# Kernel tuning notes

Hardware: AMD Instinct MI355X
Metric: run time of the kernel (lower is better)

The kernel has to match this reference:

```python
import jax, jax.numpy as jnp
import numpy as np

N = 50000
E = 800000
IN_DIM = 64
HID = 64
HEADS = 4
D = HID * HEADS  # 256
EPS = 1e-5
NEG_SLOPE = 0.2  # PyG GATConv default LeakyReLU slope


def setup_inputs() -> dict:
    key = jax.random.key(0)
    ks = jax.random.split(key, 16)
    def nrm(k, shape, s=0.05):
        return jax.random.normal(k, shape, dtype=jnp.float32) * s
    x = jax.random.normal(ks[0], (N, IN_DIM), dtype=jnp.float32)
    edge_index = jax.random.randint(ks[1], (2, E), 0, N)
    return {
        "x": x,
        "edge_index": edge_index,
        # layer 0: in=64 -> heads=4, out=64, concat -> 256
        "W0": nrm(ks[2], (IN_DIM, D)),
        "as0": nrm(ks[3], (HEADS, HID)),
        "ad0": nrm(ks[4], (HEADS, HID)),
        "b0": jnp.zeros((D,), jnp.float32),
        # layer 1: in=256 -> heads=4, out=64, concat -> 256
        "W1": nrm(ks[5], (D, D)),
        "as1": nrm(ks[6], (HEADS, HID)),
        "ad1": nrm(ks[7], (HEADS, HID)),
        "b1": jnp.zeros((D,), jnp.float32),
        # layer 2: in=256 -> heads=1, out=1, mean (concat=False)
        "W2": nrm(ks[8], (D, 1)),
        "as2": nrm(ks[9], (1, 1)),
        "ad2": nrm(ks[10], (1, 1)),
        "b2": jnp.zeros((1,), jnp.float32),
        # shared LayerNorm over 256 features
        "ln_g": jnp.ones((D,), jnp.float32),
        "ln_b": jnp.zeros((D,), jnp.float32),
    }


def _gat_conv(x, src, dst, W, a_src, a_dst, bias, concat):
    """PyG-style GATConv (self-loops already appended to src/dst)."""
    n = x.shape[0]
    H, C = a_src.shape
    h = (x @ W).reshape(n, H, C)                # [N,H,C]
    s = (h * a_src[None]).sum(-1)               # [N,H] per-node source score
    t = (h * a_dst[None]).sum(-1)               # [N,H] per-node target score
    e = jax.nn.leaky_relu(s[src] + t[dst], NEG_SLOPE)  # [E,H]
    # segment softmax over incoming edges of each destination node
    m = jax.ops.segment_max(e, dst, num_segments=n)    # [N,H]
    ex = jnp.exp(e - m[dst])
    den = jax.ops.segment_sum(ex, dst, num_segments=n)
    alpha = ex / den[dst]                       # [E,H]
    msg = h[src] * alpha[:, :, None]            # [E,H,C] gather + weight
    out = jax.ops.segment_sum(msg, dst, num_segments=n)  # [N,H,C] scatter-add
    out = out.reshape(n, H * C) if concat else out.mean(axis=1)
    return out + bias


def _layer_norm(x, g, b):
    mu = x.mean(-1, keepdims=True)
    var = ((x - mu) ** 2).mean(-1, keepdims=True)
    return (x - mu) / jnp.sqrt(var + EPS) * g + b


def reference(x, edge_index, W0, as0, ad0, b0, W1, as1, ad1, b1,
              W2, as2, ad2, b2, ln_g, ln_b):
    n = x.shape[0]
    loops = jnp.arange(n, dtype=edge_index.dtype)
    src = jnp.concatenate([edge_index[0], loops])
    dst = jnp.concatenate([edge_index[1], loops])
    h = _gat_conv(x, src, dst, W0, as0, ad0, b0, True)
    h = jax.nn.elu(_layer_norm(h, ln_g, ln_b))
    h = _gat_conv(h, src, dst, W1, as1, ad1, b1, True)
    h = jax.nn.elu(_layer_norm(h, ln_g, ln_b))
    out = _gat_conv(h, src, dst, W2, as2, ad2, b2, False)  # [N,1]
    return out
```

## Files before the change

kernel.cpp:

```cpp
#include <hip/hip_runtime.h>
#include <math.h>

constexpr float NEG_SLOPE = 0.2f;
constexpr float LN_EPS = 1e-5f;

typedef __attribute__((ext_vector_type(8))) short short8;
typedef __attribute__((ext_vector_type(4))) float f32x4;
typedef __attribute__((ext_vector_type(2))) float f32x2;

__device__ inline ushort f2bf(float f) {
    uint u = __float_as_uint(f);
    u += 0x7fffu + ((u >> 16) & 1u);
    return (ushort)(u >> 16);
}

__device__ inline float pick4(float4 v, int h) {
    float r = v.x;
    r = (h == 1) ? v.y : r;
    r = (h == 2) ? v.z : r;
    r = (h == 3) ? v.w : r;
    return r;
}

__device__ inline uchar f2q(float v) {
    int r = __builtin_amdgcn_cvt_pk_fp8_f32(v, v, 0, false);
    return (uchar)(r & 0xff);
}

__device__ inline void fma8q(const uint2& u, float q, f32x2 acc[4]) {
    f32x2 qq = {q, q};
    acc[0] += qq * __builtin_amdgcn_cvt_pk_f32_fp8(u.x, false);
    acc[1] += qq * __builtin_amdgcn_cvt_pk_f32_fp8(u.x, true);
    acc[2] += qq * __builtin_amdgcn_cvt_pk_f32_fp8(u.y, false);
    acc[3] += qq * __builtin_amdgcn_cvt_pk_f32_fp8(u.y, true);
}


__global__ void k_pre(const float* __restrict__ x,
                      const float* __restrict__ W0,
                      const float* __restrict__ W1,
                      ushort* __restrict__ Xb,
                      ushort* __restrict__ Wt0,
                      ushort* __restrict__ Wt1, int N) {
    int i = blockIdx.x * blockDim.x + threadIdx.x;
    const int nx = N * 8;
    if (i < nx) {
        float4 a = *reinterpret_cast<const float4*>(x + (size_t)i * 8);
        float4 b = *reinterpret_cast<const float4*>(x + (size_t)i * 8 + 4);
        ushort u[8] = {f2bf(a.x), f2bf(a.y), f2bf(a.z), f2bf(a.w),
                       f2bf(b.x), f2bf(b.y), f2bf(b.z), f2bf(b.w)};
        *reinterpret_cast<uint4*>(Xb + (size_t)i * 8) = *reinterpret_cast<const uint4*>(u);
        return;
    }
    i -= nx;
    if (i < 64 * 256) {
        int k = i >> 8, c = i & 255;
        Wt0[(size_t)c * 64 + k] = f2bf(W0[i]);
        return;
    }
    i -= 64 * 256;
    if (i < 256 * 256) {
        int k = i >> 8, c = i & 255;
        Wt1[(size_t)c * 256 + k] = f2bf(W1[i]);
    }
}


__global__ __launch_bounds__(1024) void k_cnt(const int* __restrict__ ei, int E, int N,
                                              int* __restrict__ bcnts) {
    __shared__ int lcnt[256];
    const int tid = threadIdx.x;
    if (tid < 256) lcnt[tid] = 0;
    __syncthreads();
    int i = blockIdx.x * 1024 + tid;
    if (i < E + N) {
        int dst = (i < E) ? ei[E + i] : (i - E);
        atomicAdd(&lcnt[dst >> 8], 1);
    }
    __syncthreads();
    if (tid < 256) bcnts[(size_t)blockIdx.x * 256 + tid] = lcnt[tid];
}

__global__ __launch_bounds__(256) void k_scanA(int* __restrict__ bcnts, int nb,
                                               int* __restrict__ wtot) {
    __shared__ int wsum[4];
    const int w = blockIdx.x;
    const int t = threadIdx.x;
    const int lane = t & 63;
    const int wv = t >> 6;
    int carry = 0;
    for (int base = 0; base < nb; base += 256) {
        int idx = base + t;
        int v = (idx < nb) ? bcnts[(size_t)idx * 256 + w] : 0;
        int sv = v;
#pragma unroll
        for (int off = 1; off < 64; off <<= 1) {
            int u = __shfl_up(sv, off);
            if (lane >= off) sv += u;
        }
        if (lane == 63) wsum[wv] = sv;
        __syncthreads();
        int add = 0;
#pragma unroll
        for (int k = 0; k < 4; ++k) add += (k < wv) ? wsum[k] : 0;
        int total = wsum[0] + wsum[1] + wsum[2] + wsum[3];
        if (idx < nb) bcnts[(size_t)idx * 256 + w] = carry + add + sv - v;
        carry += total;
        __syncthreads();
    }
    if (t == 0) wtot[w] = carry;
}

__global__ __launch_bounds__(256) void k_scanB(const int* __restrict__ wtot,
                                               int* __restrict__ wbase, int nbw) {
    __shared__ int buf[256];
    const int t = threadIdx.x;
    int v = (t < nbw) ? wtot[t] : 0;
    buf[t] = v;
    __syncthreads();
    for (int off = 1; off < 256; off <<= 1) {
        int a = (t >= off) ? buf[t - off] : 0;
        __syncthreads();
        buf[t] += a;
        __syncthreads();
    }
    if (t < nbw) wbase[t] = buf[t] - v;
}

__global__ __launch_bounds__(1024) void k_binA(const int* __restrict__ ei, int E, int N,
                                               const int* __restrict__ bcnts,
                                               const int* __restrict__ wbase,
                                               unsigned long long* __restrict__ tmp) {
    __shared__ int lcnt[256];
    __shared__ int lbase[256];
    const int tid = threadIdx.x;
    if (tid < 256) lcnt[tid] = 0;
    __syncthreads();
    int i = blockIdx.x * 1024 + tid;
    int src = 0, dst = 0, rank = 0, buc = 0;
    const bool valid = i < E + N;
    if (valid) {
        if (i < E) { src = ei[i]; dst = ei[E + i]; }
        else       { src = i - E; dst = i - E; }
        buc = dst >> 8;
        rank = atomicAdd(&lcnt[buc], 1);
    }
    __syncthreads();
    if (tid < 256)
        lbase[tid] = wbase[tid] + bcnts[(size_t)blockIdx.x * 256 + tid];
    __syncthreads();
    if (valid)
        tmp[lbase[buc] + rank] = ((unsigned long long)(uint)dst << 32) | (uint)src;
}

__global__ __launch_bounds__(256) void k_win(const unsigned long long* __restrict__ tmp,
                                             const int* __restrict__ wbase,
                                             const int* __restrict__ wtot,
                                             int nbw, int N,
                                             int* __restrict__ offs,
                                             int* __restrict__ csr) {
    __shared__ int hist[256];
    __shared__ int cur[256];
    __shared__ int buf[256];
    const int w = blockIdx.x;
    const int t = threadIdx.x;
    const int base = wbase[w];
    const int count = wtot[w];

    hist[t] = 0;
    __syncthreads();
    for (int i = t; i < count; i += 256) {
        int dst = (int)(tmp[base + i] >> 32);
        atomicAdd(&hist[dst & 255], 1);
    }
    __syncthreads();
    int v = hist[t];
    buf[t] = v;
    __syncthreads();
    for (int off = 1; off < 256; off <<= 1) {
        int a = (t >= off) ? buf[t - off] : 0;
        __syncthreads();
        buf[t] += a;
        __syncthreads();
    }
    int excl = buf[t] - v;
    cur[t] = excl;
    int node = w * 256 + t;
    if (node < N) offs[node] = base + excl;
    if (t == 0 && w == nbw - 1) offs[N] = base + count;
    __syncthreads();
    for (int i = t; i < count; i += 256) {
        unsigned long long e = tmp[base + i];
        int dst = (int)(e >> 32);
        int src = (int)(e & 0xffffffffu);
        int pos = base + atomicAdd(&cur[dst & 255], 1);
        csr[pos] = src;
    }
}


template <int K>
__global__ __launch_bounds__(256, 2) void k_gemm_mfma(
    const ushort* __restrict__ Xb, const ushort* __restrict__ Wt,
    const float* __restrict__ a_s, const float* __restrict__ a_d,
    uchar* __restrict__ h, float* __restrict__ s, float* __restrict__ t,
    int N, int nrb, int cpx, int rbpc)
{
    constexpr int KC = K / 32;
    __shared__ uchar hstage[4][16][72];

    const int tid = threadIdx.x;
    const int w = tid >> 6;
    const int l = tid & 63;
    const int lr = l & 15;
    const int lk = l >> 4;

    const int bid = blockIdx.x;
    const int xcd = bid & 7;
    const int j = bid >> 3;
    const int slice = j & 3;
    const int chunk = xcd * cpx + (j >> 2);
    const int rb0 = chunk * rbpc;
    const int rb1 = min(rb0 + rbpc, nrb);

    short8 b[4][KC];
#pragma unroll
    for (int ct = 0; ct < 4; ++ct) {
        const ushort* wp = Wt + (size_t)(slice * 64 + ct * 16 + lr) * K + lk * 8;
#pragma unroll
        for (int kc = 0; kc < KC; ++kc)
            b[ct][kc] = *reinterpret_cast<const short8*>(wp + kc * 32);
    }

    float asv[4], adv[4];
#pragma unroll
    for (int ct = 0; ct < 4; ++ct) {
        asv[ct] = a_s[slice * 64 + ct * 16 + lr];
        adv[ct] = a_d[slice * 64 + ct * 16 + lr];
    }

    for (int rb = rb0; rb < rb1; ++rb) {
        const int row0 = rb * 64 + w * 16;

        int arow = row0 + lr;
        arow = (arow < N) ? arow : (N - 1);
        const ushort* xp = Xb + (size_t)arow * K + lk * 8;
        short8 a[KC];
#pragma unroll
        for (int kc = 0; kc < KC; ++kc)
            a[kc] = *reinterpret_cast<const short8*>(xp + kc * 32);

        f32x4 acc[4];
#pragma unroll
        for (int ct = 0; ct < 4; ++ct) acc[ct] = (f32x4){0.f, 0.f, 0.f, 0.f};
#pragma unroll
        for (int ct = 0; ct < 4; ++ct)
#pragma unroll
            for (int kc = 0; kc < KC; ++kc)
                acc[ct] = __builtin_amdgcn_mfma_f32_16x16x32_bf16(a[kc], b[ct][kc], acc[ct], 0, 0, 0);

        float ps[4] = {0.f, 0.f, 0.f, 0.f}, pt[4] = {0.f, 0.f, 0.f, 0.f};
#pragma unroll
        for (int jj = 0; jj < 4; ++jj) {
#pragma unroll
            for (int ct = 0; ct < 4; ++ct) {
                float v = acc[ct][jj];
                ps[jj] = fmaf(v, asv[ct], ps[jj]);
                pt[jj] = fmaf(v, adv[ct], pt[jj]);
            }
        }
#pragma unroll
        for (int jj = 0; jj < 4; ++jj) {
#pragma unroll
            for (int o = 1; o < 16; o <<= 1) {
                ps[jj] += __shfl_xor(ps[jj], o);
                pt[jj] += __shfl_xor(pt[jj], o);
            }
        }
        if (lr == 0) {
#pragma unroll
            for (int jj = 0; jj < 4; ++jj) {
                int row = row0 + lk * 4 + jj;
                if (row < N) {
                    s[(size_t)row * 4 + slice] = ps[jj];
                    t[(size_t)row * 4 + slice] = pt[jj];
                }
            }
        }

#pragma unroll
        for (int ct = 0; ct < 4; ++ct)
#pragma unroll
            for (int jj = 0; jj < 4; ++jj)
                hstage[w][lk * 4 + jj][ct * 16 + lr] = f2q(acc[ct][jj]);
#pragma unroll
        for (int hf = 0; hf < 2; ++hf) {
            int r = (l >> 3) + hf * 8;
            int ch = l & 7;
            int grow = rb * 64 + w * 16 + r;
            uint2 v = *reinterpret_cast<const uint2*>(&hstage[w][r][ch * 8]);
            if (grow < N)
                *reinterpret_cast<uint2*>(h + (size_t)grow * 256 + slice * 64 + ch * 8) = v;
        }
    }
}


template <bool FUSE_W2>
__global__ __launch_bounds__(256) void k_agg_ln_elu(
    const int* __restrict__ offs, const int* __restrict__ csr,
    const float* __restrict__ s, const float* __restrict__ t,
    const uchar* __restrict__ h, const float* __restrict__ bias,
    const float* __restrict__ lng, const float* __restrict__ lnb,
    ushort* __restrict__ Y, const float* __restrict__ W2,
    float* __restrict__ h2, int N)
{
    __shared__ float p_s[4][2][32][4];
    __shared__ int off_s[4][2][32];

    const int tid = threadIdx.x;
    const int wid = tid >> 6;
    const int lane = tid & 63;
    const int half = lane >> 5;
    const int lh = lane & 31;
    const int n = blockIdx.x * 8 + wid * 2 + half;
    if (n >= N) return;
    const int head = lh >> 3;
    const int c0 = lh * 8;

    const float4 t4 = *reinterpret_cast<const float4*>(t + (size_t)n * 4);
    const int beg = offs[n], end = offs[n + 1];

    float4 m4 = make_float4(-1e30f, -1e30f, -1e30f, -1e30f);
    float4 den4 = make_float4(0.f, 0.f, 0.f, 0.f);
    f32x2 acc2[4];
#pragma unroll
    for (int c = 0; c < 4; ++c) acc2[c] = (f32x2){0.f, 0.f};

    const uchar* hb = h + lh * 8;
    float* pp = &p_s[wid][half][0][0];
    int* op = &off_s[wid][half][0];

    for (int base = beg; base < end; base += 32) {
        const int cnt = min(32, end - base);
        int src = 0;
        float4 e4 = make_float4(-1e30f, -1e30f, -1e30f, -1e30f);
        if (lh < cnt) {
            src = csr[base + lh];
            float4 sv = *reinterpret_cast<const float4*>(s + (size_t)src * 4);
            float ex = sv.x + t4.x, ey = sv.y + t4.y, ez = sv.z + t4.z, ew = sv.w + t4.w;
            e4.x = fmaxf(ex, NEG_SLOPE * ex);
            e4.y = fmaxf(ey, NEG_SLOPE * ey);
            e4.z = fmaxf(ez, NEG_SLOPE * ez);
            e4.w = fmaxf(ew, NEG_SLOPE * ew);
        }
        float4 bm = e4;
#pragma unroll
        for (int off = 1; off < 32; off <<= 1) {
            bm.x = fmaxf(bm.x, __shfl_xor(bm.x, off));
            bm.y = fmaxf(bm.y, __shfl_xor(bm.y, off));
            bm.z = fmaxf(bm.z, __shfl_xor(bm.z, off));
            bm.w = fmaxf(bm.w, __shfl_xor(bm.w, off));
        }
        float4 newm = make_float4(fmaxf(m4.x, bm.x), fmaxf(m4.y, bm.y),
                                  fmaxf(m4.z, bm.z), fmaxf(m4.w, bm.w));
        float4 sc4 = make_float4(__expf(m4.x - newm.x), __expf(m4.y - newm.y),
                                 __expf(m4.z - newm.z), __expf(m4.w - newm.w));
        m4 = newm;
        float sch = pick4(sc4, head);
        f32x2 sch2 = {sch, sch};
#pragma unroll
        for (int c = 0; c < 4; ++c) acc2[c] *= sch2;
        float4 p4 = make_float4(__expf(e4.x - newm.x), __expf(e4.y - newm.y),
                                __expf(e4.z - newm.z), __expf(e4.w - newm.w));
        den4.x = den4.x * sc4.x + p4.x;
        den4.y = den4.y * sc4.y + p4.y;
        den4.z = den4.z * sc4.z + p4.z;
        den4.w = den4.w * sc4.w + p4.w;

        *reinterpret_cast<float4*>(&p_s[wid][half][lh][0]) = p4;
        op[lh] = src << 8;
        asm volatile("s_waitcnt lgkmcnt(0)" ::: "memory");

        for (int j0 = 0; j0 < cnt; j0 += 4) {
            int o0 = op[j0 + 0];
            int o1 = op[j0 + 1];
            int o2 = op[j0 + 2];
            int o3 = op[j0 + 3];
            float q0 = pp[(j0 + 0) * 4 + head];
            float q1 = pp[(j0 + 1) * 4 + head];
            float q2 = pp[(j0 + 2) * 4 + head];
            float q3 = pp[(j0 + 3) * 4 + head];
            uint2 u0 = *reinterpret_cast<const uint2*>(hb + o0);
            uint2 u1 = *reinterpret_cast<const uint2*>(hb + o1);
            uint2 u2 = *reinterpret_cast<const uint2*>(hb + o2);
            uint2 u3 = *reinterpret_cast<const uint2*>(hb + o3);
            fma8q(u0, q0, acc2);
            fma8q(u1, q1, acc2);
            fma8q(u2, q2, acc2);
            fma8q(u3, q3, acc2);
        }
    }

    float4 dsum = den4;
#pragma unroll
    for (int off = 1; off < 32; off <<= 1) {
        dsum.x += __shfl_xor(dsum.x, off);
        dsum.y += __shfl_xor(dsum.y, off);
        dsum.z += __shfl_xor(dsum.z, off);
        dsum.w += __shfl_xor(dsum.w, off);
    }
    const float inv = 1.0f / pick4(dsum, head);
    float4 bv0 = *reinterpret_cast<const float4*>(bias + c0);
    float4 bv1 = *reinterpret_cast<const float4*>(bias + c0 + 4);
    float v[8];
    v[0] = acc2[0][0] * inv + bv0.x; v[1] = acc2[0][1] * inv + bv0.y;
    v[2] = acc2[1][0] * inv + bv0.z; v[3] = acc2[1][1] * inv + bv0.w;
    v[4] = acc2[2][0] * inv + bv1.x; v[5] = acc2[2][1] * inv + bv1.y;
    v[6] = acc2[3][0] * inv + bv1.z; v[7] = acc2[3][1] * inv + bv1.w;

    float sum = 0.f;
#pragma unroll
    for (int c = 0; c < 8; ++c) sum += v[c];
#pragma unroll
    for (int off = 1; off < 32; off <<= 1) sum += __shfl_xor(sum, off);
    float mu = sum * (1.0f / 256.0f);
    float d[8], vs = 0.f;
#pragma unroll
    for (int c = 0; c < 8; ++c) { d[c] = v[c] - mu; vs = fmaf(d[c], d[c], vs); }
#pragma unroll
    for (int off = 1; off < 32; off <<= 1) vs += __shfl_xor(vs, off);
    float rstd = rsqrtf(vs * (1.0f / 256.0f) + LN_EPS);
    float4 gv0 = *reinterpret_cast<const float4*>(lng + c0);
    float4 gv1 = *reinterpret_cast<const float4*>(lng + c0 + 4);
    float4 bb0 = *reinterpret_cast<const float4*>(lnb + c0);
    float4 bb1 = *reinterpret_cast<const float4*>(lnb + c0 + 4);
    float g[8] = {gv0.x, gv0.y, gv0.z, gv0.w, gv1.x, gv1.y, gv1.z, gv1.w};
    float bbv[8] = {bb0.x, bb0.y, bb0.z, bb0.w, bb1.x, bb1.y, bb1.z, bb1.w};
    float o[8];
#pragma unroll
    for (int c = 0; c < 8; ++c) {
        float val = fmaf(d[c] * rstd, g[c], bbv[c]);
        o[c] = (val > 0.f) ? val : (__expf(val) - 1.0f);
    }

    if (FUSE_W2) {
        float4 wv0 = *reinterpret_cast<const float4*>(W2 + c0);
        float4 wv1 = *reinterpret_cast<const float4*>(W2 + c0 + 4);
        float wv[8] = {wv0.x, wv0.y, wv0.z, wv0.w, wv1.x, wv1.y, wv1.z, wv1.w};
        float p = 0.f;
#pragma unroll
        for (int c = 0; c < 8; ++c) p = fmaf(o[c], wv[c], p);
#pragma unroll
        for (int off = 1; off < 32; off <<= 1) p += __shfl_xor(p, off);
        if (lh == 0) h2[n] = p;
    } else {
        ushort yo[8];
#pragma unroll
        for (int c = 0; c < 8; ++c) yo[c] = f2bf(o[c]);
        *reinterpret_cast<uint4*>(Y + (size_t)n * 256 + c0) =
            *reinterpret_cast<const uint4*>(yo);
    }
}


__global__ __launch_bounds__(256) void k_agg2(
    const int* __restrict__ offs, const int* __restrict__ csr,
    const float* __restrict__ h2,
    const float* __restrict__ as2, const float* __restrict__ ad2,
    const float* __restrict__ b2, float* __restrict__ out, int N)
{
    const int tid = threadIdx.x;
    const int wid = tid >> 6;
    const int lane = tid & 63;
    const int quarter = lane >> 4;
    const int lq = lane & 15;
    const int n = blockIdx.x * 16 + wid * 4 + quarter;
    if (n >= N) return;
    const float asv = as2[0], adv = ad2[0];
    const float tval = adv * h2[n];
    const int beg = offs[n], end = offs[n + 1];

    float m = -1e30f, den = 0.f, num = 0.f;
    for (int i = beg + lq; i < end; i += 16) {
        float hv = h2[csr[i]];
        float e = fmaf(asv, hv, tval);
        e = fmaxf(e, NEG_SLOPE * e);
        float nm = fmaxf(m, e);
        float sc = __expf(m - nm);
        float p = __expf(e - nm);
        den = den * sc + p;
        num = fmaf(num, sc, p * hv);
        m = nm;
    }
#pragma unroll
    for (int o = 1; o < 16; o <<= 1) {
        float m2 = __shfl_xor(m, o);
        float d2 = __shfl_xor(den, o);
        float n2 = __shfl_xor(num, o);
        float nm = fmaxf(m, m2);
        float sA = __expf(m - nm);
        float sB = __expf(m2 - nm);
        den = den * sA + d2 * sB;
        num = num * sA + n2 * sB;
        m = nm;
    }
    if (lq == 0) out[n] = num / den + b2[0];
}


extern "C" void kernel_launch(void* const* d_in, const int* in_sizes, int n_in,
                              void* d_out, int out_size, void* d_ws, size_t ws_size,
                              hipStream_t stream) {
    const float* x   = (const float*)d_in[0];
    const int*   ei  = (const int*)d_in[1];
    const float* W0  = (const float*)d_in[2];
    const float* as0 = (const float*)d_in[3];
    const float* ad0 = (const float*)d_in[4];
    const float* b0  = (const float*)d_in[5];
    const float* W1  = (const float*)d_in[6];
    const float* as1 = (const float*)d_in[7];
    const float* ad1 = (const float*)d_in[8];
    const float* b1  = (const float*)d_in[9];
    const float* W2  = (const float*)d_in[10];
    const float* as2 = (const float*)d_in[11];
    const float* ad2 = (const float*)d_in[12];
    const float* b2  = (const float*)d_in[13];
    const float* lng = (const float*)d_in[14];
    const float* lnb = (const float*)d_in[15];

    const int N = in_sizes[0] / 64;
    const int E = in_sizes[1] / 2;
    const int TOT = E + N;
    const int NBW = (N + 255) / 256;
    const int NBC = (TOT + 1023) / 1024;

    char* w = (char*)d_ws;
    auto alloc = [&](size_t bytes) -> void* {
        void* p = (void*)w;
        w += (bytes + 255) & ~(size_t)255;
        return p;
    };
    int*    offs   = (int*)alloc(sizeof(int) * (N + 1));
    int*    csr    = (int*)alloc(sizeof(int) * TOT);
    int*    bcnts  = (int*)alloc(sizeof(int) * (size_t)NBC * 256);
    int*    wtot   = (int*)alloc(sizeof(int) * 256);
    int*    wbase  = (int*)alloc(sizeof(int) * 256);
    unsigned long long* tmp = (unsigned long long*)alloc(sizeof(unsigned long long) * TOT);
    float*  sbuf   = (float*)alloc(sizeof(float) * N * 4);
    float*  tbuf   = (float*)alloc(sizeof(float) * N * 4);
    ushort* Xb     = (ushort*)alloc(sizeof(ushort) * (size_t)N * 64);
    ushort* Wt0    = (ushort*)alloc(sizeof(ushort) * 256 * 64);
    ushort* Wt1    = (ushort*)alloc(sizeof(ushort) * 256 * 256);
    uchar*  hq     = (uchar*)alloc(sizeof(uchar) * (size_t)N * 256);
    ushort* Yb     = (ushort*)alloc(sizeof(ushort) * (size_t)N * 256);
    float*  h2     = (float*)alloc(sizeof(float) * N);
    float*  out    = (float*)d_out;

    const int pre_tot = N * 8 + 64 * 256 + 256 * 256;
    k_pre<<<(pre_tot + 255) / 256, 256, 0, stream>>>(x, W0, W1, Xb, Wt0, Wt1, N);

    k_cnt<<<NBC, 1024, 0, stream>>>(ei, E, N, bcnts);
    k_scanA<<<NBW, 256, 0, stream>>>(bcnts, NBC, wtot);
    k_scanB<<<1, 256, 0, stream>>>(wtot, wbase, NBW);
    k_binA<<<NBC, 1024, 0, stream>>>(ei, E, N, bcnts, wbase, tmp);
    k_win<<<NBW, 256, 0, stream>>>(tmp, wbase, wtot, NBW, N, offs, csr);

    const int nrb = (N + 63) / 64;
    const int cpx = 25;
    const int chunks = 8 * cpx;
    const int rbpc = (nrb + chunks - 1) / chunks;
    const int gemm_grid = chunks * 4;
    const int node_grid8 = (N + 7) / 8;
    const int node_grid16 = (N + 15) / 16;

    k_gemm_mfma<64><<<gemm_grid, 256, 0, stream>>>(Xb, Wt0, as0, ad0, hq, sbuf, tbuf,
                                                   N, nrb, cpx, rbpc);
    k_agg_ln_elu<false><<<node_grid8, 256, 0, stream>>>(offs, csr, sbuf, tbuf, hq,
                                                        b0, lng, lnb, Yb, nullptr, nullptr, N);
    k_gemm_mfma<256><<<gemm_grid, 256, 0, stream>>>(Yb, Wt1, as1, ad1, hq, sbuf, tbuf,
                                                    N, nrb, cpx, rbpc);
    k_agg_ln_elu<true><<<node_grid8, 256, 0, stream>>>(offs, csr, sbuf, tbuf, hq,
                                                       b1, lng, lnb, nullptr, W2, h2, N);
    k_agg2<<<node_grid16, 256, 0, stream>>>(offs, csr, h2, as2, ad2, b2, out, N);
}
```

Before: 184.7 us.

## Replace online softmax with global per-head max bound; fuse edge count into preprocess

The GEMM kernels now reduce a global per-head maximum of the source scores and publish it through an atomicMax on order-preserving float keys. The aggregation kernels use leaky_relu(max_s + t_dst) as a fixed softmax shift, which removes the per-chunk max shuffles, rescale exponentials and accumulator rescaling. Separately, the destination-count pass is folded into the preprocessing kernel, and the binning kernels move from 1024-thread to 256-thread blocks. A fixed upper-bound shift can underflow exponentials when scores vary widely, which risks accuracy on other inputs. It also adds a memset and a cross-kernel dependency.

```diff
diff --git a/kernel.cpp b/kernel.cpp
--- a/kernel.cpp
+++ b/kernel.cpp
@@ -14,12 +14,13 @@
     return (ushort)(u >> 16);
 }
 
-__device__ inline float pick4(float4 v, int h) {
-    float r = v.x;
-    r = (h == 1) ? v.y : r;
-    r = (h == 2) ? v.z : r;
-    r = (h == 3) ? v.w : r;
-    return r;
+__device__ inline uint fkey(float f) {
+    uint u = __float_as_uint(f);
+    return (u & 0x80000000u) ? ~u : (u | 0x80000000u);
+}
+__device__ inline float funkey(uint k) {
+    uint u = (k & 0x80000000u) ? (k ^ 0x80000000u) : ~k;
+    return __uint_as_float(u);
 }
 
 __device__ inline uchar f2q(float v) {
@@ -36,13 +37,31 @@
 }
 
 
-__global__ void k_pre(const float* __restrict__ x,
-                      const float* __restrict__ W0,
-                      const float* __restrict__ W1,
-                      ushort* __restrict__ Xb,
-                      ushort* __restrict__ Wt0,
-                      ushort* __restrict__ Wt1, int N) {
-    int i = blockIdx.x * blockDim.x + threadIdx.x;
+__global__ __launch_bounds__(256) void k_pre(
+    const float* __restrict__ x,
+    const float* __restrict__ W0,
+    const float* __restrict__ W1,
+    const int* __restrict__ ei,
+    ushort* __restrict__ Xb,
+    ushort* __restrict__ Wt0,
+    ushort* __restrict__ Wt1,
+    int* __restrict__ bcnts, int N, int E, int NBC) {
+    __shared__ int lcnt[256];
+    const int tid = threadIdx.x;
+    const int TOT = E + N;
+    if ((int)blockIdx.x < NBC) {
+        lcnt[tid] = 0;
+        __syncthreads();
+        int gi = blockIdx.x * 256 + tid;
+        if (gi < TOT) {
+            int dst = (gi < E) ? ei[E + gi] : (gi - E);
+            atomicAdd(&lcnt[dst >> 8], 1);
+        }
+        __syncthreads();
+        bcnts[(size_t)blockIdx.x * 256 + tid] = lcnt[tid];
+        return;
+    }
+    int i = (blockIdx.x - NBC) * 256 + tid;
     const int nx = N * 8;
     if (i < nx) {
         float4 a = *reinterpret_cast<const float4*>(x + (size_t)i * 8);
@@ -65,21 +84,6 @@
     }
 }
 
-
-__global__ __launch_bounds__(1024) void k_cnt(const int* __restrict__ ei, int E, int N,
-                                              int* __restrict__ bcnts) {
-    __shared__ int lcnt[256];
-    const int tid = threadIdx.x;
-    if (tid < 256) lcnt[tid] = 0;
-    __syncthreads();
-    int i = blockIdx.x * 1024 + tid;
-    if (i < E + N) {
-        int dst = (i < E) ? ei[E + i] : (i - E);
-        atomicAdd(&lcnt[dst >> 8], 1);
-    }
-    __syncthreads();
-    if (tid < 256) bcnts[(size_t)blockIdx.x * 256 + tid] = lcnt[tid];
-}
 
 __global__ __launch_bounds__(256) void k_scanA(int* __restrict__ bcnts, int nb,
                                                int* __restrict__ wtot) {
@@ -124,19 +128,19 @@
         buf[t] += a;
         __syncthreads();
     }
-    if (t < nbw) wbase[t] = buf[t] - v;
-}
-
-__global__ __launch_bounds__(1024) void k_binA(const int* __restrict__ ei, int E, int N,
-                                               const int* __restrict__ bcnts,
-                                               const int* __restrict__ wbase,
-                                               unsigned long long* __restrict__ tmp) {
+    wbase[t] = buf[t] - v;
+}
+
+__global__ __launch_bounds__(256) void k_binA(const int* __restrict__ ei, int E, int N,
+                                              const int* __restrict__ bcnts,
+                                              const int* __restrict__ wbase,
+                                              unsigned long long* __restrict__ tmp) {
     __shared__ int lcnt[256];
     __shared__ int lbase[256];
     const int tid = threadIdx.x;
-    if (tid < 256) lcnt[tid] = 0;
-    __syncthreads();
-    int i = blockIdx.x * 1024 + tid;
+    lcnt[tid] = 0;
+    __syncthreads();
+    int i = blockIdx.x * 256 + tid;
     int src = 0, dst = 0, rank = 0, buc = 0;
     const bool valid = i < E + N;
     if (valid) {
@@ -146,8 +150,7 @@
         rank = atomicAdd(&lcnt[buc], 1);
     }
     __syncthreads();
-    if (tid < 256)
-        lbase[tid] = wbase[tid] + bcnts[(size_t)blockIdx.x * 256 + tid];
+    lbase[tid] = wbase[tid] + bcnts[(size_t)blockIdx.x * 256 + tid];
     __syncthreads();
     if (valid)
         tmp[lbase[buc] + rank] = ((unsigned long long)(uint)dst << 32) | (uint)src;
@@ -204,10 +207,11 @@
     const ushort* __restrict__ Xb, const ushort* __restrict__ Wt,
     const float* __restrict__ a_s, const float* __restrict__ a_d,
     uchar* __restrict__ h, float* __restrict__ s, float* __restrict__ t,
-    int N, int nrb, int cpx, int rbpc)
+    uint* __restrict__ gkey, int N, int nrb, int cpx, int rbpc)
 {
     constexpr int KC = K / 32;
     __shared__ uchar hstage[4][16][72];
+    __shared__ float wmax[4];
 
     const int tid = threadIdx.x;
     const int w = tid >> 6;
@@ -239,6 +243,8 @@
         adv[ct] = a_d[slice * 64 + ct * 16 + lr];
     }
 
+    float blockmax = -1e30f;
+
     for (int rb = rb0; rb < rb1; ++rb) {
         const int row0 = rb * 64 + w * 16;
 
@@ -287,6 +293,10 @@
                 }
             }
         }
+        float mx = fmaxf(fmaxf(ps[0], ps[1]), fmaxf(ps[2], ps[3]));
+        mx = fmaxf(mx, __shfl_xor(mx, 16));
+        mx = fmaxf(mx, __shfl_xor(mx, 32));
+        blockmax = fmaxf(blockmax, mx);
 
 #pragma unroll
         for (int ct = 0; ct < 4; ++ct)
@@ -303,6 +313,13 @@
                 *reinterpret_cast<uint2*>(h + (size_t)grow * 256 + slice * 64 + ch * 8) = v;
         }
     }
+
+    if (l == 0) wmax[w] = blockmax;
+    __syncthreads();
+    if (tid == 0) {
+        float m = fmaxf(fmaxf(wmax[0], wmax[1]), fmaxf(wmax[2], wmax[3]));
+        atomicMax(&gkey[slice], fkey(m));
+    }
 }
 
 
@@ -310,7 +327,8 @@
 __global__ __launch_bounds__(256) void k_agg_ln_elu(
     const int* __restrict__ offs, const int* __restrict__ csr,
     const float* __restrict__ s, const float* __restrict__ t,
-    const uchar* __restrict__ h, const float* __restrict__ bias,
+    const uchar* __restrict__ h, const uint* __restrict__ gkey,
+    const float* __restrict__ bias,
     const float* __restrict__ lng, const float* __restrict__ lnb,
     ushort* __restrict__ Y, const float* __restrict__ W2,
     float* __restrict__ h2, int N)
@@ -329,9 +347,17 @@
     const int c0 = lh * 8;
 
     const float4 t4 = *reinterpret_cast<const float4*>(t + (size_t)n * 4);
+    uint4 gk4 = *reinterpret_cast<const uint4*>(gkey);
+    float4 Mh;
+    {
+        float mx;
+        mx = funkey(gk4.x) + t4.x; Mh.x = fmaxf(mx, NEG_SLOPE * mx);
+        mx = funkey(gk4.y) + t4.y; Mh.y = fmaxf(mx, NEG_SLOPE * mx);
+        mx = funkey(gk4.z) + t4.z; Mh.z = fmaxf(mx, NEG_SLOPE * mx);
+        mx = funkey(gk4.w) + t4.w; Mh.w = fmaxf(mx, NEG_SLOPE * mx);
+    }
     const int beg = offs[n], end = offs[n + 1];
 
-    float4 m4 = make_float4(-1e30f, -1e30f, -1e30f, -1e30f);
     float4 den4 = make_float4(0.f, 0.f, 0.f, 0.f);
     f32x2 acc2[4];
 #pragma unroll
@@ -344,39 +370,20 @@
     for (int base = beg; base < end; base += 32) {
         const int cnt = min(32, end - base);
         int src = 0;
-        float4 e4 = make_float4(-1e30f, -1e30f, -1e30f, -1e30f);
+        float4 p4 = make_float4(0.f, 0.f, 0.f, 0.f);
         if (lh < cnt) {
             src = csr[base + lh];
             float4 sv = *reinterpret_cast<const float4*>(s + (size_t)src * 4);
-            float ex = sv.x + t4.x, ey = sv.y + t4.y, ez = sv.z + t4.z, ew = sv.w + t4.w;
-            e4.x = fmaxf(ex, NEG_SLOPE * ex);
-            e4.y = fmaxf(ey, NEG_SLOPE * ey);
-            e4.z = fmaxf(ez, NEG_SLOPE * ez);
-            e4.w = fmaxf(ew, NEG_SLOPE * ew);
-        }
-        float4 bm = e4;
-#pragma unroll
-        for (int off = 1; off < 32; off <<= 1) {
-            bm.x = fmaxf(bm.x, __shfl_xor(bm.x, off));
-            bm.y = fmaxf(bm.y, __shfl_xor(bm.y, off));
-            bm.z = fmaxf(bm.z, __shfl_xor(bm.z, off));
-            bm.w = fmaxf(bm.w, __shfl_xor(bm.w, off));
-        }
-        float4 newm = make_float4(fmaxf(m4.x, bm.x), fmaxf(m4.y, bm.y),
-                                  fmaxf(m4.z, bm.z), fmaxf(m4.w, bm.w));
-        float4 sc4 = make_float4(__expf(m4.x - newm.x), __expf(m4.y - newm.y),
-                                 __expf(m4.z - newm.z), __expf(m4.w - newm.w));
-        m4 = newm;
-        float sch = pick4(sc4, head);
-        f32x2 sch2 = {sch, sch};
-#pragma unroll
-        for (int c = 0; c < 4; ++c) acc2[c] *= sch2;
-        float4 p4 = make_float4(__expf(e4.x - newm.x), __expf(e4.y - newm.y),
-                                __expf(e4.z - newm.z), __expf(e4.w - newm.w));
-        den4.x = den4.x * sc4.x + p4.x;
-        den4.y = den4.y * sc4.y + p4.y;
-        den4.z = den4.z * sc4.z + p4.z;
-        den4.w = den4.w * sc4.w + p4.w;
+            float ex = sv.x + t4.x; ex = fmaxf(ex, NEG_SLOPE * ex);
+            float ey = sv.y + t4.y; ey = fmaxf(ey, NEG_SLOPE * ey);
+            float ez = sv.z + t4.z; ez = fmaxf(ez, NEG_SLOPE * ez);
+            float ew = sv.w + t4.w; ew = fmaxf(ew, NEG_SLOPE * ew);
+            p4.x = __expf(ex - Mh.x);
+            p4.y = __expf(ey - Mh.y);
+            p4.z = __expf(ez - Mh.z);
+            p4.w = __expf(ew - Mh.w);
+        }
+        den4.x += p4.x; den4.y += p4.y; den4.z += p4.z; den4.w += p4.w;
 
         *reinterpret_cast<float4*>(&p_s[wid][half][lh][0]) = p4;
         op[lh] = src << 8;
@@ -410,7 +417,11 @@
         dsum.z += __shfl_xor(dsum.z, off);
         dsum.w += __shfl_xor(dsum.w, off);
     }
-    const float inv = 1.0f / pick4(dsum, head);
+    float dh = dsum.x;
+    dh = (head == 1) ? dsum.y : dh;
+    dh = (head == 2) ? dsum.z : dh;
+    dh = (head == 3) ? dsum.w : dh;
+    const float inv = 1.0f / dh;
     float4 bv0 = *reinterpret_cast<const float4*>(bias + c0);
     float4 bv1 = *reinterpret_cast<const float4*>(bias + c0 + 4);
     float v[8];
@@ -533,7 +544,7 @@
     const int E = in_sizes[1] / 2;
     const int TOT = E + N;
     const int NBW = (N + 255) / 256;
-    const int NBC = (TOT + 1023) / 1024;
+    const int NBC = (TOT + 255) / 256;
 
     char* w = (char*)d_ws;
     auto alloc = [&](size_t bytes) -> void* {
@@ -546,6 +557,7 @@
     int*    bcnts  = (int*)alloc(sizeof(int) * (size_t)NBC * 256);
     int*    wtot   = (int*)alloc(sizeof(int) * 256);
     int*    wbase  = (int*)alloc(sizeof(int) * 256);
+    uint*   gkeys  = (uint*)alloc(sizeof(uint) * 8);
     unsigned long long* tmp = (unsigned long long*)alloc(sizeof(unsigned long long) * TOT);
     float*  sbuf   = (float*)alloc(sizeof(float) * N * 4);
     float*  tbuf   = (float*)alloc(sizeof(float) * N * 4);
@@ -557,13 +569,15 @@
     float*  h2     = (float*)alloc(sizeof(float) * N);
     float*  out    = (float*)d_out;
 
+    hipMemsetAsync(gkeys, 0, sizeof(uint) * 8, stream);
+
     const int pre_tot = N * 8 + 64 * 256 + 256 * 256;
-    k_pre<<<(pre_tot + 255) / 256, 256, 0, stream>>>(x, W0, W1, Xb, Wt0, Wt1, N);
-
-    k_cnt<<<NBC, 1024, 0, stream>>>(ei, E, N, bcnts);
+    const int pre_grid = NBC + (pre_tot + 255) / 256;
+    k_pre<<<pre_grid, 256, 0, stream>>>(x, W0, W1, ei, Xb, Wt0, Wt1, bcnts, N, E, NBC);
+
     k_scanA<<<NBW, 256, 0, stream>>>(bcnts, NBC, wtot);
     k_scanB<<<1, 256, 0, stream>>>(wtot, wbase, NBW);
-    k_binA<<<NBC, 1024, 0, stream>>>(ei, E, N, bcnts, wbase, tmp);
+    k_binA<<<NBC, 256, 0, stream>>>(ei, E, N, bcnts, wbase, tmp);
     k_win<<<NBW, 256, 0, stream>>>(tmp, wbase, wtot, NBW, N, offs, csr);
 
     const int nrb = (N + 63) / 64;
@@ -575,12 +589,12 @@
     const int node_grid16 = (N + 15) / 16;
 
     k_gemm_mfma<64><<<gemm_grid, 256, 0, stream>>>(Xb, Wt0, as0, ad0, hq, sbuf, tbuf,
-                                                   N, nrb, cpx, rbpc);
-    k_agg_ln_elu<false><<<node_grid8, 256, 0, stream>>>(offs, csr, sbuf, tbuf, hq,
+                                                   gkeys, N, nrb, cpx, rbpc);
+    k_agg_ln_elu<false><<<node_grid8, 256, 0, stream>>>(offs, csr, sbuf, tbuf, hq, gkeys,
                                                         b0, lng, lnb, Yb, nullptr, nullptr, N);
     k_gemm_mfma<256><<<gemm_grid, 256, 0, stream>>>(Yb, Wt1, as1, ad1, hq, sbuf, tbuf,
-                                                    N, nrb, cpx, rbpc);
-    k_agg_ln_elu<true><<<node_grid8, 256, 0, stream>>>(offs, csr, sbuf, tbuf, hq,
+                                                    gkeys + 4, N, nrb, cpx, rbpc);
+    k_agg_ln_elu<true><<<node_grid8, 256, 0, stream>>>(offs, csr, sbuf, tbuf, hq, gkeys + 4,
                                                        b1, lng, lnb, nullptr, W2, h2, N);
     k_agg2<<<node_grid16, 256, 0, stream>>>(offs, csr, h2, as2, ad2, b2, out, N);
 }
```

Result: slower. 200.3 us (+8.5%).
